# Kernel tuning notes

Measured on AMD Instinct MI355X. Metric: run time of the kernel, lower is better.

Reference implementation:

```python
import jax, jax.numpy as jnp
import numpy as np

B, S, D_IN, D_OUT = 4, 2048, 2048, 8192


def setup_inputs() -> dict:
    key = jax.random.key(0)
    k1, k2 = jax.random.split(key)
    x = jax.random.normal(k1, (B, S, D_IN), dtype=jnp.float32)
    weight = jax.random.normal(k2, (D_OUT, D_IN), dtype=jnp.float32) * 0.02
    alpha = jnp.float32(1.0)
    bias = jnp.zeros((D_OUT,), dtype=jnp.float32)
    return {"x": x, "weight": weight, "alpha": alpha, "bias": bias}


def reference(x, weight, alpha, bias):
    # Ternary quantization: delta = 0.7 * mean(|w|); w_q in {-1,0,1} * alpha
    delta = 0.7 * jnp.mean(jnp.abs(weight))
    w_t = jnp.where(weight > delta, jnp.float32(1.0),
                    jnp.where(weight < -delta, jnp.float32(-1.0), jnp.float32(0.0)))
    w_q = w_t * alpha  # [out, in]
    # F.linear: x @ w_q^T + bias
    return jnp.einsum('bsd,od->bso', x, w_q) + bias
```

## Files before the change

kernel.cpp:

```cpp
#include <hip/hip_runtime.h>
#include <hip/hip_bf16.h>
#include <stdint.h>

typedef __attribute__((ext_vector_type(4))) int i32x4;
typedef __attribute__((ext_vector_type(16))) int i32x16;
typedef signed char s8;

#define M_TOT 8192
#define N_TOT 8192
#define K_TOT 2048
#define W_COUNT (N_TOT * K_TOT)
#define X_COUNT (M_TOT * K_TOT)

__global__ void tl_reduce(const float* __restrict__ w, const float* __restrict__ x,
                          double* __restrict__ wsum, float* __restrict__ xmax) {
    const int b = blockIdx.x;
    if (b < 1024) {
        const int tid = b * 256 + threadIdx.x;
        const float4* w4 = (const float4*)w;
        double s = 0.0;
        for (int i = tid; i < W_COUNT / 4; i += 1024 * 256) {
            float4 v = w4[i];
            s += (double)fabsf(v.x) + (double)fabsf(v.y) + (double)fabsf(v.z) + (double)fabsf(v.w);
        }
        #pragma unroll
        for (int off = 32; off > 0; off >>= 1) s += __shfl_down(s, off);
        __shared__ double red[4];
        if ((threadIdx.x & 63) == 0) red[threadIdx.x >> 6] = s;
        __syncthreads();
        if (threadIdx.x == 0) wsum[b] = (red[0] + red[1]) + (red[2] + red[3]);
    } else {
        const int tid = (b - 1024) * 256 + threadIdx.x;
        const float4* x4 = (const float4*)x;
        float m = 0.0f;
        for (int i = tid; i < X_COUNT / 4; i += 1024 * 256) {
            float4 v = x4[i];
            m = fmaxf(m, fmaxf(fmaxf(fabsf(v.x), fabsf(v.y)), fmaxf(fabsf(v.z), fabsf(v.w))));
        }
        #pragma unroll
        for (int off = 32; off > 0; off >>= 1) m = fmaxf(m, __shfl_down(m, off));
        __shared__ float redm[4];
        if ((threadIdx.x & 63) == 0) redm[threadIdx.x >> 6] = m;
        __syncthreads();
        if (threadIdx.x == 0) xmax[b - 1024] = fmaxf(fmaxf(redm[0], redm[1]), fmaxf(redm[2], redm[3]));
    }
}

__global__ void tl_finalize(const double* __restrict__ wsum, const float* __restrict__ xmax,
                            const float* __restrict__ alpha,
                            double* __restrict__ delta, float* __restrict__ qp) {
    const int t = threadIdx.x;
    double s = (wsum[t] + wsum[t + 256]) + (wsum[t + 512] + wsum[t + 768]);
    float m = fmaxf(fmaxf(xmax[t], xmax[t + 256]), fmaxf(xmax[t + 512], xmax[t + 768]));
    #pragma unroll
    for (int off = 32; off > 0; off >>= 1) {
        s += __shfl_down(s, off);
        m = fmaxf(m, __shfl_down(m, off));
    }
    __shared__ double rs[4];
    __shared__ float rm[4];
    if ((t & 63) == 0) { rs[t >> 6] = s; rm[t >> 6] = m; }
    __syncthreads();
    if (t == 0) {
        *delta = 0.7 * (((rs[0] + rs[1]) + (rs[2] + rs[3])) / (double)W_COUNT);
        float mm = fmaxf(fmaxf(rm[0], rm[1]), fmaxf(rm[2], rm[3]));
        qp[0] = 127.0f / mm;
        qp[1] = alpha[0] * (mm / 127.0f);
    }
}

__global__ void tl_quant(const float* __restrict__ w, const float* __restrict__ x,
                         const double* __restrict__ delta_p, const float* __restrict__ qp,
                         s8* __restrict__ wb, s8* __restrict__ xb) {
    const int b = blockIdx.x;
    if (b < 4096) {
        const double d = *delta_p;
        const int i = (b * 256 + threadIdx.x) * 16;
        union { s8 c[16]; i32x4 v; } o;
        #pragma unroll
        for (int j = 0; j < 16; j += 4) {
            float4 v = *(const float4*)(w + i + j);
            float f[4] = {v.x, v.y, v.z, v.w};
            #pragma unroll
            for (int r = 0; r < 4; ++r) {
                double wd = (double)f[r];
                o.c[j + r] = wd > d ? 1 : (wd < -d ? -1 : 0);
            }
        }
        *(i32x4*)(wb + i) = o.v;
    } else {
        const float inv = qp[0];
        const int i = ((b - 4096) * 256 + threadIdx.x) * 16;
        union { s8 c[16]; i32x4 v; } o;
        #pragma unroll
        for (int j = 0; j < 16; j += 4) {
            float4 v = *(const float4*)(x + i + j);
            float f[4] = {v.x, v.y, v.z, v.w};
            #pragma unroll
            for (int r = 0; r < 4; ++r) {
                int q = (int)__builtin_rintf(f[r] * inv);
                q = q > 127 ? 127 : (q < -127 ? -127 : q);
                o.c[j + r] = (s8)q;
            }
        }
        *(i32x4*)(xb + i) = o.v;
    }
}


#define SB    __builtin_amdgcn_sched_barrier(0)
#define BARR  __builtin_amdgcn_s_barrier()
#define LGKM4 asm volatile("s_waitcnt lgkmcnt(4)" ::: "memory")
#define LGKM0 asm volatile("s_waitcnt lgkmcnt(0)" ::: "memory")
#define VMW(N) asm volatile("s_waitcnt vmcnt(" #N ")" ::: "memory")

#define GLDS(SRC, DOFF) __builtin_amdgcn_global_load_lds(                      \
    (const __attribute__((address_space(1))) void*)(SRC),                      \
    (__attribute__((address_space(3))) void*)(lds + (DOFF)), 16, 0, 0)

#define RD4(AR, BR, S, KK) do {                                                \
    _Pragma("unroll") for (int m_ = 0; m_ < 2; ++m_)                           \
        AR[m_] = *(const i32x4*)(lds + (S) * 16384 + wrOff + m_ * 2048 +       \
                                 (lrd ^ ((KK) * 32)));                         \
    _Pragma("unroll") for (int n_ = 0; n_ < 2; ++n_)                           \
        BR[n_] = *(const i32x4*)(lds + 49152 + (S) * 8192 + wcOff + n_ * 2048 + \
                                 (lrd ^ ((KK) * 32)));                         \
} while (0)

#define MM4(AR, BR) do {                                                       \
    _Pragma("unroll") for (int m_ = 0; m_ < 2; ++m_)                           \
    _Pragma("unroll") for (int n_ = 0; n_ < 2; ++n_)                           \
        acc[m_][n_] = __builtin_amdgcn_mfma_i32_32x32x32_i8(                   \
            AR[m_], BR[n_], acc[m_][n_], 0, 0, 0);                             \
} while (0)

#define STG_A(SS, KOFF) do {                                                   \
    GLDS(aSrc + (KOFF), (SS) * 16384 + L);                                     \
    GLDS(aSrc + (KOFF) + (size_t)128 * K_TOT, (SS) * 16384 + 8192 + L);        \
} while (0)
#define STG_B(SS, KOFF)                                                        \
    GLDS(bSrc + (KOFF), 49152 + (SS) * 8192 + L)

#define KTILE(S, SN, SG, KOFF, DOSTG, GATE, DONEXT) do {                       \
    RD4(aO, bO, S, 1);                                                         \
    LGKM4; SB;                                                                 \
    MM4(aE, bE);                                                               \
    if (DOSTG) { STG_A(SG, KOFF); STG_B(SG, KOFF); }                           \
    LGKM0; SB;                                                                 \
    GATE; SB;                                                                  \
    BARR;                                                                      \
    if (DONEXT) RD4(aE, bE, SN, 0);                                            \
    MM4(aO, bO);                                                               \
} while (0)

__global__ __launch_bounds__(512, 4) void tl_gemm_i8(
    const s8* __restrict__ A, const s8* __restrict__ Bm,
    const float* __restrict__ qp, const float* __restrict__ bias,
    float* __restrict__ C) {
    __shared__ __attribute__((aligned(128))) char lds[73728];

    const int t = threadIdx.x;
    const int wid = t >> 6;
    const int l = t & 63;
    const int wr = wid >> 1;
    const int wc = wid & 1;

    const int bid = blockIdx.x;
    const int xc = bid & 7;
    const int j = bid >> 3;
    const int tm = xc * 4 + ((j >> 4) & 3);
    const int tn = (j & 15) + (j >> 6) * 16;
    const int row0 = tm * 256, col0 = tn * 128;

    const int L = t * 16;
    const int off = L ^ (((L >> 7) & 3) << 4);
    const int sr = off >> 6;
    const int kb = off & 63;
    const s8* aSrc = A + (size_t)(row0 + sr) * K_TOT + kb;
    const s8* bSrc = Bm + (size_t)(col0 + sr) * K_TOT + kb;

    const int rl = l & 31, kg = l >> 5;
    const int lrd = rl * 64 + ((kg ^ ((rl >> 1) & 3)) << 4);
    const int wrOff = wr * 4096;
    const int wcOff = wc * 4096;

    i32x16 acc[2][2] = {};
    i32x4 aE[2], bE[2], aO[2], bO[2];

    STG_A(0, 0); STG_B(0, 0);
    STG_A(1, 64); STG_B(1, 64);
    VMW(3); SB; BARR;
    RD4(aE, bE, 0, 0);

    int koff = 128;
    #pragma unroll 1
    for (int i = 0; i < 10; ++i) {
        KTILE(0, 1, 2, koff, 1, VMW(3), 1); koff += 64;
        KTILE(1, 2, 0, koff, 1, VMW(3), 1); koff += 64;
        KTILE(2, 0, 1, koff, 1, VMW(3), 1); koff += 64;
    }
    KTILE(0, 1, 0, 0, 0, VMW(0), 1);
    KTILE(1, 0, 0, 0, 0, (void)0, 0);

    const float osc = qp[1];
    #pragma unroll
    for (int m_ = 0; m_ < 2; ++m_) {
        const int crow = row0 + wr * 64 + m_ * 32 + kg * 4;
        #pragma unroll
        for (int n_ = 0; n_ < 2; ++n_) {
            const int ccol = col0 + wc * 64 + n_ * 32 + rl;
            const float bv = bias[ccol];
            #pragma unroll
            for (int r = 0; r < 16; ++r) {
                const int row = crow + (r & 3) + 8 * (r >> 2);
                C[(size_t)row * N_TOT + ccol] = (float)acc[m_][n_][r] * osc + bv;
            }
        }
    }
}

extern "C" void kernel_launch(void* const* d_in, const int* in_sizes, int n_in,
                              void* d_out, int out_size, void* d_ws, size_t ws_size,
                              hipStream_t stream) {
    const float* x     = (const float*)d_in[0];
    const float* wgt   = (const float*)d_in[1];
    const float* alpha = (const float*)d_in[2];
    const float* bias  = (const float*)d_in[3];
    float* out = (float*)d_out;

    char* ws = (char*)d_ws;
    double* wsum = (double*)ws;
    float* xmax  = (float*)(ws + 8192);
    double* delta = (double*)(ws + 12288);
    float* qp     = (float*)(ws + 12304);
    s8* xb = (s8*)(ws + 16384);
    s8* wb = (s8*)(ws + 16384 + (size_t)X_COUNT);

    tl_reduce<<<2048, 256, 0, stream>>>(wgt, x, wsum, xmax);
    tl_finalize<<<1, 256, 0, stream>>>(wsum, xmax, alpha, delta, qp);
    tl_quant<<<8192, 256, 0, stream>>>(wgt, x, delta, qp, wb, xb);
    tl_gemm_i8<<<(M_TOT / 256) * (N_TOT / 128), 512, 0, stream>>>(xb, wb, qp, bias, out);
}
```

Measured before the change: 206.8 us.

## Shrink GEMM block tile to 128x128 with 2x4 warp layout for occupancy

Changes the int8 GEMM block tile from 256x128 to 128x128, rearranges the eight waves as 2x4 so each wave computes a 64x32 sub-tile, and cuts the LDS ring from 72KB to 48KB. The launch bound rises to 6 blocks per CU and the grid doubles. The aim is higher occupancy and better latency hiding. In exchange, arithmetic intensity per LDS read falls (3 reads for 2 MFMAs instead of 4 for 4) and global traffic for the A/B tiles increases.

```diff
diff --git a/kernel.cpp b/kernel.cpp
--- a/kernel.cpp
+++ b/kernel.cpp
@@ -110,7 +110,7 @@
 
 #define SB    __builtin_amdgcn_sched_barrier(0)
 #define BARR  __builtin_amdgcn_s_barrier()
-#define LGKM4 asm volatile("s_waitcnt lgkmcnt(4)" ::: "memory")
+#define LGKM3 asm volatile("s_waitcnt lgkmcnt(3)" ::: "memory")
 #define LGKM0 asm volatile("s_waitcnt lgkmcnt(0)" ::: "memory")
 #define VMW(N) asm volatile("s_waitcnt vmcnt(" #N ")" ::: "memory")
 
@@ -118,59 +118,53 @@
     (const __attribute__((address_space(1))) void*)(SRC),                      \
     (__attribute__((address_space(3))) void*)(lds + (DOFF)), 16, 0, 0)
 
-#define RD4(AR, BR, S, KK) do {                                                \
-    _Pragma("unroll") for (int m_ = 0; m_ < 2; ++m_)                           \
-        AR[m_] = *(const i32x4*)(lds + (S) * 16384 + wrOff + m_ * 2048 +       \
-                                 (lrd ^ ((KK) * 32)));                         \
-    _Pragma("unroll") for (int n_ = 0; n_ < 2; ++n_)                           \
-        BR[n_] = *(const i32x4*)(lds + 49152 + (S) * 8192 + wcOff + n_ * 2048 + \
-                                 (lrd ^ ((KK) * 32)));                         \
+#define RD3(AR, BR_, S, KK) do {                                               \
+    AR[0] = *(const i32x4*)(lds + (S) * 8192 + wrOff + 0 * 2048 +              \
+                            (lrd ^ ((KK) * 32)));                              \
+    AR[1] = *(const i32x4*)(lds + (S) * 8192 + wrOff + 1 * 2048 +              \
+                            (lrd ^ ((KK) * 32)));                              \
+    BR_ = *(const i32x4*)(lds + 24576 + (S) * 8192 + wcOff +                   \
+                          (lrd ^ ((KK) * 32)));                                \
 } while (0)
 
-#define MM4(AR, BR) do {                                                       \
-    _Pragma("unroll") for (int m_ = 0; m_ < 2; ++m_)                           \
-    _Pragma("unroll") for (int n_ = 0; n_ < 2; ++n_)                           \
-        acc[m_][n_] = __builtin_amdgcn_mfma_i32_32x32x32_i8(                   \
-            AR[m_], BR[n_], acc[m_][n_], 0, 0, 0);                             \
+#define MM2(AR, BR_) do {                                                      \
+    acc[0] = __builtin_amdgcn_mfma_i32_32x32x32_i8(AR[0], BR_, acc[0], 0, 0, 0); \
+    acc[1] = __builtin_amdgcn_mfma_i32_32x32x32_i8(AR[1], BR_, acc[1], 0, 0, 0); \
 } while (0)
 
-#define STG_A(SS, KOFF) do {                                                   \
-    GLDS(aSrc + (KOFF), (SS) * 16384 + L);                                     \
-    GLDS(aSrc + (KOFF) + (size_t)128 * K_TOT, (SS) * 16384 + 8192 + L);        \
-} while (0)
-#define STG_B(SS, KOFF)                                                        \
-    GLDS(bSrc + (KOFF), 49152 + (SS) * 8192 + L)
+#define STG_A(SS, KOFF) GLDS(aSrc + (KOFF), (SS) * 8192 + L)
+#define STG_B(SS, KOFF) GLDS(bSrc + (KOFF), 24576 + (SS) * 8192 + L)
 
 #define KTILE(S, SN, SG, KOFF, DOSTG, GATE, DONEXT) do {                       \
-    RD4(aO, bO, S, 1);                                                         \
-    LGKM4; SB;                                                                 \
-    MM4(aE, bE);                                                               \
+    RD3(aO, bO, S, 1);                                                         \
+    LGKM3; SB;                                                                 \
+    MM2(aE, bE);                                                               \
     if (DOSTG) { STG_A(SG, KOFF); STG_B(SG, KOFF); }                           \
     LGKM0; SB;                                                                 \
     GATE; SB;                                                                  \
     BARR;                                                                      \
-    if (DONEXT) RD4(aE, bE, SN, 0);                                            \
-    MM4(aO, bO);                                                               \
+    if (DONEXT) RD3(aE, bE, SN, 0);                                            \
+    MM2(aO, bO);                                                               \
 } while (0)
 
-__global__ __launch_bounds__(512, 4) void tl_gemm_i8(
+__global__ __launch_bounds__(512, 6) void tl_gemm_i8(
     const s8* __restrict__ A, const s8* __restrict__ Bm,
     const float* __restrict__ qp, const float* __restrict__ bias,
     float* __restrict__ C) {
-    __shared__ __attribute__((aligned(128))) char lds[73728];
+    __shared__ __attribute__((aligned(128))) char lds[49152];
 
     const int t = threadIdx.x;
     const int wid = t >> 6;
     const int l = t & 63;
-    const int wr = wid >> 1;
-    const int wc = wid & 1;
+    const int wr = wid >> 2;
+    const int wc = wid & 3;
 
     const int bid = blockIdx.x;
     const int xc = bid & 7;
     const int j = bid >> 3;
-    const int tm = xc * 4 + ((j >> 4) & 3);
-    const int tn = (j & 15) + (j >> 6) * 16;
-    const int row0 = tm * 256, col0 = tn * 128;
+    const int tm = xc * 8 + ((j >> 4) & 7);
+    const int tn = (j & 15) + ((j >> 7) << 4);
+    const int row0 = tm * 128, col0 = tn * 128;
 
     const int L = t * 16;
     const int off = L ^ (((L >> 7) & 3) << 4);
@@ -182,39 +176,36 @@
     const int rl = l & 31, kg = l >> 5;
     const int lrd = rl * 64 + ((kg ^ ((rl >> 1) & 3)) << 4);
     const int wrOff = wr * 4096;
-    const int wcOff = wc * 4096;
-
-    i32x16 acc[2][2] = {};
-    i32x4 aE[2], bE[2], aO[2], bO[2];
+    const int wcOff = wc * 2048;
+
+    i32x16 acc[2] = {};
+    i32x4 aE[2], aO[2], bE, bO;
 
     STG_A(0, 0); STG_B(0, 0);
     STG_A(1, 64); STG_B(1, 64);
-    VMW(3); SB; BARR;
-    RD4(aE, bE, 0, 0);
+    VMW(2); SB; BARR;
+    RD3(aE, bE, 0, 0);
 
     int koff = 128;
     #pragma unroll 1
     for (int i = 0; i < 10; ++i) {
-        KTILE(0, 1, 2, koff, 1, VMW(3), 1); koff += 64;
-        KTILE(1, 2, 0, koff, 1, VMW(3), 1); koff += 64;
-        KTILE(2, 0, 1, koff, 1, VMW(3), 1); koff += 64;
+        KTILE(0, 1, 2, koff, 1, VMW(2), 1); koff += 64;
+        KTILE(1, 2, 0, koff, 1, VMW(2), 1); koff += 64;
+        KTILE(2, 0, 1, koff, 1, VMW(2), 1); koff += 64;
     }
     KTILE(0, 1, 0, 0, 0, VMW(0), 1);
     KTILE(1, 0, 0, 0, 0, (void)0, 0);
 
     const float osc = qp[1];
+    const int ccol = col0 + wc * 32 + rl;
+    const float bv = bias[ccol];
     #pragma unroll
     for (int m_ = 0; m_ < 2; ++m_) {
         const int crow = row0 + wr * 64 + m_ * 32 + kg * 4;
         #pragma unroll
-        for (int n_ = 0; n_ < 2; ++n_) {
-            const int ccol = col0 + wc * 64 + n_ * 32 + rl;
-            const float bv = bias[ccol];
-            #pragma unroll
-            for (int r = 0; r < 16; ++r) {
-                const int row = crow + (r & 3) + 8 * (r >> 2);
-                C[(size_t)row * N_TOT + ccol] = (float)acc[m_][n_][r] * osc + bv;
-            }
+        for (int r = 0; r < 16; ++r) {
+            const int row = crow + (r & 3) + 8 * (r >> 2);
+            C[(size_t)row * N_TOT + ccol] = (float)acc[m_][r] * osc + bv;
         }
     }
 }
@@ -239,5 +230,5 @@
     tl_reduce<<<2048, 256, 0, stream>>>(wgt, x, wsum, xmax);
     tl_finalize<<<1, 256, 0, stream>>>(wsum, xmax, alpha, delta, qp);
     tl_quant<<<8192, 256, 0, stream>>>(wgt, x, delta, qp, wb, xb);
-    tl_gemm_i8<<<(M_TOT / 256) * (N_TOT / 128), 512, 0, stream>>>(xb, wb, qp, bias, out);
-}
+    tl_gemm_i8<<<(M_TOT / 128) * (N_TOT / 128), 512, 0, stream>>>(xb, wb, qp, bias, out);
+}
```

After: 235.0 us. 13.6% more time.
